# Optimization experiments

Measured on AMD Instinct MI355X. Metric: run time of the kernel, lower is better.

The kernel has to match this reference:

```python
import jax, jax.numpy as jnp
import numpy as np
import math

NEG_INF = -1e30  # stand-in for float('-inf'); softmax/logsumexp treat it identically


def _fnoise(x):
    # factorized NoisyNet transform f(x) = sign(x) * sqrt(|x|)
    return jnp.sign(x) * jnp.sqrt(jnp.abs(x))


def setup_inputs() -> dict:
    B, T, D, E = 4, 4096, 2048, 16
    key = jax.random.key(0)
    ks = jax.random.split(key, 6)
    sigma_init = 0.4 / math.sqrt(D)  # sigma_zero / sqrt(in_features)
    return {
        "mh_output": jax.random.normal(ks[0], (B, T, D), dtype=jnp.float32),
        "weight": jax.random.normal(ks[1], (E, D), dtype=jnp.float32) * 0.02,
        "sigma_weight": jnp.full((E, D), sigma_init, dtype=jnp.float32),
        "bias": jax.random.normal(ks[2], (E,), dtype=jnp.float32) * 0.02,
        "sigma_bias": jnp.full((E,), sigma_init, dtype=jnp.float32),
        "eps_in": jax.random.normal(ks[3], (D,), dtype=jnp.float32),
        "eps_out": jax.random.normal(ks[4], (E,), dtype=jnp.float32),
    }


def reference(mh_output, weight, sigma_weight, bias, sigma_bias, eps_in, eps_out):
    top_k = 2
    E = weight.shape[0]

    # NoisyFactorizedLinear: W' = W + sigma_W * (f(eps_out) f(eps_in)^T)
    f_in = _fnoise(eps_in)            # [D]
    f_out = _fnoise(eps_out)          # [E]
    w_noisy = weight + sigma_weight * (f_out[:, None] * f_in[None, :])  # [E, D]
    b_noisy = bias + sigma_bias * f_out                                 # [E]
    logits = jnp.einsum("btd,ed->bte", mh_output, w_noisy) + b_noisy    # [B,T,E]
    # dropout(p=0.125) is identity in eval mode

    top_vals, indices = jax.lax.top_k(logits, top_k)                    # [B,T,k]
    # scatter top-k back into a -inf-filled tensor == mask of selected experts
    keep = jnp.sum(jax.nn.one_hot(indices, E, dtype=jnp.bool_), axis=-2)  # [B,T,E]
    sparse_logits = jnp.where(keep, logits, NEG_INF)

    router_output = jax.nn.softmax(sparse_logits, axis=-1)

    # z-loss: mean(logsumexp(sparse_logits, -1)^2); only top-k entries survive
    lse = jax.scipy.special.logsumexp(top_vals, axis=-1)                # [B,T]
    z_loss = jnp.mean(lse ** 2)

    return router_output, indices, z_loss
```

## Files before the change

### kernel.cpp

```cpp
#include <hip/hip_runtime.h>
#include <math.h>

#define NROWS 16384
#define DDIM  2048
#define NEXP  16
#define RBLOCKS 512
#define WPB 8
#define ZN (RBLOCKS * WPB)

__device__ __forceinline__ float fnoise(float x) {
    return copysignf(sqrtf(fabsf(x)), x);
}

__device__ __forceinline__ void async_copy16(const float4* g, float4* l) {
    __builtin_amdgcn_global_load_lds(
        (const __attribute__((address_space(1))) void*)g,
        (__attribute__((address_space(3))) void*)l, 16, 0, 0);
}


__global__ void prep_kernel(const float* __restrict__ weight,
                            const float* __restrict__ sigma_weight,
                            const float* __restrict__ bias,
                            const float* __restrict__ sigma_bias,
                            const float* __restrict__ eps_in,
                            const float* __restrict__ eps_out,
                            float* __restrict__ w_noisy,
                            float* __restrict__ b_noisy) {
    int idx = blockIdx.x * blockDim.x + threadIdx.x;
    int e = idx >> 11;
    int d = idx & (DDIM - 1);
    float fi = fnoise(eps_in[d]);
    float fo = fnoise(eps_out[e]);
    w_noisy[idx] = weight[idx] + sigma_weight[idx] * fo * fi;
    if (idx < NEXP) {
        b_noisy[idx] = bias[idx] + sigma_bias[idx] * fnoise(eps_out[idx]);
    }
}

__global__ __launch_bounds__(512, 2) void router_kernel(
        const float* __restrict__ x,
        const float* __restrict__ w_noisy,
        const float* __restrict__ b_noisy,
        float* __restrict__ out_router,
        float* __restrict__ out_idx,
        float* __restrict__ zpart) {
    __shared__ float4 wlds[NEXP * 512];

    const int tid  = threadIdx.x;
    const int wv   = tid >> 6;
    const int lane = tid & 63;

    const int rowBase = blockIdx.x * 32 + wv * 4;
    const float4* xr0 = (const float4*)(x + (size_t)(rowBase + 0) * DDIM);
    const float4* xr1 = (const float4*)(x + (size_t)(rowBase + 1) * DDIM);
    const float4* xr2 = (const float4*)(x + (size_t)(rowBase + 2) * DDIM);
    const float4* xr3 = (const float4*)(x + (size_t)(rowBase + 3) * DDIM);
    const float4* wsrc = (const float4*)w_noisy;

    float acc[64];
    #pragma unroll
    for (int i = 0; i < 64; ++i) acc[i] = 0.0f;

    float4 xbuf[3][4];

    #pragma unroll
    for (int j = 0; j < 16; ++j) {
        int fb = j * 512 + wv * 64;
        async_copy16(wsrc + fb + lane, &wlds[fb]);
    }
    xbuf[0][0] = xr0[lane];       xbuf[0][1] = xr1[lane];
    xbuf[0][2] = xr2[lane];       xbuf[0][3] = xr3[lane];
    xbuf[1][0] = xr0[64 + lane];  xbuf[1][1] = xr1[64 + lane];
    xbuf[1][2] = xr2[64 + lane];  xbuf[1][3] = xr3[64 + lane];
    __syncthreads();

    #pragma unroll
    for (int c = 0; c < 8; ++c) {
        const int cur = c % 3;
        const int pre = (c + 2) % 3;
        if (c < 6) {
            int p = (c + 2) * 64 + lane;
            xbuf[pre][0] = xr0[p];
            xbuf[pre][1] = xr1[p];
            xbuf[pre][2] = xr2[p];
            xbuf[pre][3] = xr3[p];
        }
        #pragma unroll
        for (int e = 0; e < 16; ++e) {
            float4 w = wlds[e * 512 + c * 64 + lane];
            float s0 = acc[0 * 16 + e];
            float s1 = acc[1 * 16 + e];
            float s2 = acc[2 * 16 + e];
            float s3 = acc[3 * 16 + e];
            s0 = fmaf(xbuf[cur][0].x, w.x, s0); s0 = fmaf(xbuf[cur][0].y, w.y, s0);
            s0 = fmaf(xbuf[cur][0].z, w.z, s0); s0 = fmaf(xbuf[cur][0].w, w.w, s0);
            s1 = fmaf(xbuf[cur][1].x, w.x, s1); s1 = fmaf(xbuf[cur][1].y, w.y, s1);
            s1 = fmaf(xbuf[cur][1].z, w.z, s1); s1 = fmaf(xbuf[cur][1].w, w.w, s1);
            s2 = fmaf(xbuf[cur][2].x, w.x, s2); s2 = fmaf(xbuf[cur][2].y, w.y, s2);
            s2 = fmaf(xbuf[cur][2].z, w.z, s2); s2 = fmaf(xbuf[cur][2].w, w.w, s2);
            s3 = fmaf(xbuf[cur][3].x, w.x, s3); s3 = fmaf(xbuf[cur][3].y, w.y, s3);
            s3 = fmaf(xbuf[cur][3].z, w.z, s3); s3 = fmaf(xbuf[cur][3].w, w.w, s3);
            acc[0 * 16 + e] = s0;
            acc[1 * 16 + e] = s1;
            acc[2 * 16 + e] = s2;
            acc[3 * 16 + e] = s3;
        }
    }

    #pragma unroll
    for (int half = 32; half >= 1; half >>= 1) {
        #pragma unroll
        for (int i = 0; i < half; ++i) {
            bool hi = (lane & half) != 0;
            float keep = hi ? acc[i + half] : acc[i];
            float send = hi ? acc[i] : acc[i + half];
            float recv = __shfl_xor(send, half, 64);
            acc[i] = keep + recv;
        }
    }

    const int e = lane & 15;
    const int r = lane >> 4;
    const int row = rowBase + r;
    float logit = acc[0] + b_noisy[e];

    float m1 = logit; int i1 = e;
    #pragma unroll
    for (int off = 8; off >= 1; off >>= 1) {
        float om = __shfl_xor(m1, off, 64);
        int   oi = __shfl_xor(i1, off, 64);
        if (om > m1 || (om == m1 && oi < i1)) { m1 = om; i1 = oi; }
    }
    float v2 = (e == i1) ? -3.4e38f : logit;
    float m2 = v2; int i2 = e;
    #pragma unroll
    for (int off = 8; off >= 1; off >>= 1) {
        float om = __shfl_xor(m2, off, 64);
        int   oi = __shfl_xor(i2, off, 64);
        if (om > m2 || (om == m2 && oi < i2)) { m2 = om; i2 = oi; }
    }

    float t = expf(m2 - m1);
    float p1 = 1.0f / (1.0f + t);
    float val = (e == i1) ? p1 : ((e == i2) ? t * p1 : 0.0f);
    out_router[(size_t)rowBase * NEXP + lane] = val;

    if (e < 2) {
        out_idx[(size_t)row * 2 + e] = (float)((e == 0) ? i1 : i2);
    }

    float zv = 0.0f;
    if (e == 0) {
        float lse = m1 + log1pf(t);
        zv = lse * lse;
    }
    zv += __shfl_xor(zv, 16, 64);
    zv += __shfl_xor(zv, 32, 64);
    if (lane == 0) {
        zpart[blockIdx.x * WPB + wv] = zv;
    }
}

__global__ void finalize_kernel(const float* __restrict__ zpart,
                                float* __restrict__ out) {
    __shared__ float ws4[4];
    int tid = threadIdx.x;
    float s = 0.0f;
    for (int i = tid; i < ZN; i += 256) s += zpart[i];
    #pragma unroll
    for (int off = 32; off >= 1; off >>= 1) s += __shfl_xor(s, off, 64);
    if ((tid & 63) == 0) ws4[tid >> 6] = s;
    __syncthreads();
    if (tid == 0) {
        float total = ws4[0] + ws4[1] + ws4[2] + ws4[3];
        out[NROWS * NEXP + NROWS * 2] = total * (1.0f / (float)NROWS);
    }
}

extern "C" void kernel_launch(void* const* d_in, const int* in_sizes, int n_in,
                              void* d_out, int out_size, void* d_ws, size_t ws_size,
                              hipStream_t stream) {
    const float* mh      = (const float*)d_in[0];
    const float* weight  = (const float*)d_in[1];
    const float* sigw    = (const float*)d_in[2];
    const float* bias    = (const float*)d_in[3];
    const float* sigb    = (const float*)d_in[4];
    const float* eps_in  = (const float*)d_in[5];
    const float* eps_out = (const float*)d_in[6];

    float* out      = (float*)d_out;
    float* w_noisy  = (float*)d_ws;
    float* b_noisy  = w_noisy + NEXP * DDIM;
    float* zpart    = w_noisy + 32800;

    prep_kernel<<<(NEXP * DDIM) / 256, 256, 0, stream>>>(
        weight, sigw, bias, sigb, eps_in, eps_out, w_noisy, b_noisy);

    router_kernel<<<RBLOCKS, 512, 0, stream>>>(
        mh, w_noisy, b_noisy, out, out + NROWS * NEXP, zpart);

    finalize_kernel<<<1, 256, 0, stream>>>(zpart, out);
}
```

Baseline: 212.5 us.

## Process eight rows per wave with split-D weight staging in LDS

Each wave now handles 8 rows instead of 4, so each LDS weight read is reused across twice as many rows, and the grid is halved to 256 blocks. The weight matrix is staged in two halves of the D dimension: the second half is loaded asynchronously while the first is being consumed, which halves the LDS footprint. The x loads are restructured into a two-buffer ping-pong inside a non-unrolled outer loop. The cost is 128 accumulators per thread, which raises register pressure, and fewer blocks for a memory-bound stream over a large x.

```diff
diff --git a/kernel.cpp b/kernel.cpp
--- a/kernel.cpp
+++ b/kernel.cpp
@@ -4,7 +4,7 @@
 #define NROWS 16384
 #define DDIM  2048
 #define NEXP  16
-#define RBLOCKS 512
+#define RBLOCKS 256
 #define WPB 8
 #define ZN (RBLOCKS * WPB)
 
@@ -45,66 +45,74 @@
         float* __restrict__ out_router,
         float* __restrict__ out_idx,
         float* __restrict__ zpart) {
-    __shared__ float4 wlds[NEXP * 512];
+    __shared__ float4 wlds[2 * NEXP * 256];
 
     const int tid  = threadIdx.x;
     const int wv   = tid >> 6;
     const int lane = tid & 63;
 
-    const int rowBase = blockIdx.x * 32 + wv * 4;
-    const float4* xr0 = (const float4*)(x + (size_t)(rowBase + 0) * DDIM);
-    const float4* xr1 = (const float4*)(x + (size_t)(rowBase + 1) * DDIM);
-    const float4* xr2 = (const float4*)(x + (size_t)(rowBase + 2) * DDIM);
-    const float4* xr3 = (const float4*)(x + (size_t)(rowBase + 3) * DDIM);
+    const int rowBase = blockIdx.x * 64 + wv * 8;
+    const float4* xbase = (const float4*)x + (size_t)rowBase * 512;
     const float4* wsrc = (const float4*)w_noisy;
 
-    float acc[64];
-    #pragma unroll
-    for (int i = 0; i < 64; ++i) acc[i] = 0.0f;
-
-    float4 xbuf[3][4];
-
-    #pragma unroll
-    for (int j = 0; j < 16; ++j) {
+    float acc[128];
+    #pragma unroll
+    for (int i = 0; i < 128; ++i) acc[i] = 0.0f;
+
+    float4 xa[8], xb[8];
+
+    #pragma unroll
+    for (int j = 0; j < 8; ++j) {
         int fb = j * 512 + wv * 64;
-        async_copy16(wsrc + fb + lane, &wlds[fb]);
-    }
-    xbuf[0][0] = xr0[lane];       xbuf[0][1] = xr1[lane];
-    xbuf[0][2] = xr2[lane];       xbuf[0][3] = xr3[lane];
-    xbuf[1][0] = xr0[64 + lane];  xbuf[1][1] = xr1[64 + lane];
-    xbuf[1][2] = xr2[64 + lane];  xbuf[1][3] = xr3[64 + lane];
+        async_copy16(wsrc + (fb >> 8) * 512 + (fb & 255) + lane, &wlds[fb]);
+    }
+    #pragma unroll
+    for (int r = 0; r < 8; ++r) xa[r] = xbase[r * 512 + lane];
     __syncthreads();
 
     #pragma unroll
-    for (int c = 0; c < 8; ++c) {
-        const int cur = c % 3;
-        const int pre = (c + 2) % 3;
-        if (c < 6) {
-            int p = (c + 2) * 64 + lane;
-            xbuf[pre][0] = xr0[p];
-            xbuf[pre][1] = xr1[p];
-            xbuf[pre][2] = xr2[p];
-            xbuf[pre][3] = xr3[p];
-        }
+    for (int j = 0; j < 8; ++j) {
+        int fb = j * 512 + wv * 64;
+        async_copy16(wsrc + (fb >> 8) * 512 + 256 + (fb & 255) + lane,
+                     &wlds[4096 + fb]);
+    }
+
+    #pragma unroll 1
+    for (int c2 = 0; c2 < 4; ++c2) {
+        if (c2 == 2) __syncthreads();
+        const float4* wb = wlds + (c2 >> 1) * 4096 + (c2 & 1) * 128;
+        const int pe = 2 * c2 * 64 + lane;
+
+        #pragma unroll
+        for (int r = 0; r < 8; ++r) xb[r] = xbase[r * 512 + pe + 64];
+
         #pragma unroll
         for (int e = 0; e < 16; ++e) {
-            float4 w = wlds[e * 512 + c * 64 + lane];
-            float s0 = acc[0 * 16 + e];
-            float s1 = acc[1 * 16 + e];
-            float s2 = acc[2 * 16 + e];
-            float s3 = acc[3 * 16 + e];
-            s0 = fmaf(xbuf[cur][0].x, w.x, s0); s0 = fmaf(xbuf[cur][0].y, w.y, s0);
-            s0 = fmaf(xbuf[cur][0].z, w.z, s0); s0 = fmaf(xbuf[cur][0].w, w.w, s0);
-            s1 = fmaf(xbuf[cur][1].x, w.x, s1); s1 = fmaf(xbuf[cur][1].y, w.y, s1);
-            s1 = fmaf(xbuf[cur][1].z, w.z, s1); s1 = fmaf(xbuf[cur][1].w, w.w, s1);
-            s2 = fmaf(xbuf[cur][2].x, w.x, s2); s2 = fmaf(xbuf[cur][2].y, w.y, s2);
-            s2 = fmaf(xbuf[cur][2].z, w.z, s2); s2 = fmaf(xbuf[cur][2].w, w.w, s2);
-            s3 = fmaf(xbuf[cur][3].x, w.x, s3); s3 = fmaf(xbuf[cur][3].y, w.y, s3);
-            s3 = fmaf(xbuf[cur][3].z, w.z, s3); s3 = fmaf(xbuf[cur][3].w, w.w, s3);
-            acc[0 * 16 + e] = s0;
-            acc[1 * 16 + e] = s1;
-            acc[2 * 16 + e] = s2;
-            acc[3 * 16 + e] = s3;
+            float4 w = wb[e * 256 + lane];
+            #pragma unroll
+            for (int r = 0; r < 8; ++r) {
+                float s = acc[r * 16 + e];
+                s = fmaf(xa[r].x, w.x, s); s = fmaf(xa[r].y, w.y, s);
+                s = fmaf(xa[r].z, w.z, s); s = fmaf(xa[r].w, w.w, s);
+                acc[r * 16 + e] = s;
+            }
+        }
+
+        if (c2 < 3) {
+            #pragma unroll
+            for (int r = 0; r < 8; ++r) xa[r] = xbase[r * 512 + pe + 128];
+        }
+
+        #pragma unroll
+        for (int e = 0; e < 16; ++e) {
+            float4 w = wb[e * 256 + 64 + lane];
+            #pragma unroll
+            for (int r = 0; r < 8; ++r) {
+                float s = acc[r * 16 + e];
+                s = fmaf(xb[r].x, w.x, s); s = fmaf(xb[r].y, w.y, s);
+                s = fmaf(xb[r].z, w.z, s); s = fmaf(xb[r].w, w.w, s);
+                acc[r * 16 + e] = s;
+            }
         }
     }
 
@@ -115,46 +123,51 @@
             bool hi = (lane & half) != 0;
             float keep = hi ? acc[i + half] : acc[i];
             float send = hi ? acc[i] : acc[i + half];
-            float recv = __shfl_xor(send, half, 64);
-            acc[i] = keep + recv;
+            acc[i] = keep + __shfl_xor(send, half, 64);
+            float keep2 = hi ? acc[64 + i + half] : acc[64 + i];
+            float send2 = hi ? acc[64 + i] : acc[64 + i + half];
+            acc[64 + i] = keep2 + __shfl_xor(send2, half, 64);
         }
     }
 
     const int e = lane & 15;
-    const int r = lane >> 4;
-    const int row = rowBase + r;
-    float logit = acc[0] + b_noisy[e];
-
-    float m1 = logit; int i1 = e;
-    #pragma unroll
-    for (int off = 8; off >= 1; off >>= 1) {
-        float om = __shfl_xor(m1, off, 64);
-        int   oi = __shfl_xor(i1, off, 64);
-        if (om > m1 || (om == m1 && oi < i1)) { m1 = om; i1 = oi; }
-    }
-    float v2 = (e == i1) ? -3.4e38f : logit;
-    float m2 = v2; int i2 = e;
-    #pragma unroll
-    for (int off = 8; off >= 1; off >>= 1) {
-        float om = __shfl_xor(m2, off, 64);
-        int   oi = __shfl_xor(i2, off, 64);
-        if (om > m2 || (om == m2 && oi < i2)) { m2 = om; i2 = oi; }
-    }
-
-    float t = expf(m2 - m1);
-    float p1 = 1.0f / (1.0f + t);
-    float val = (e == i1) ? p1 : ((e == i2) ? t * p1 : 0.0f);
-    out_router[(size_t)rowBase * NEXP + lane] = val;
-
-    if (e < 2) {
-        out_idx[(size_t)row * 2 + e] = (float)((e == 0) ? i1 : i2);
-    }
-
+    const float bn = b_noisy[e];
     float zv = 0.0f;
-    if (e == 0) {
-        float lse = m1 + log1pf(t);
-        zv = lse * lse;
-    }
+
+    #pragma unroll
+    for (int s = 0; s < 2; ++s) {
+        float logit = acc[s * 64] + bn;
+
+        float m1 = logit; int i1 = e;
+        #pragma unroll
+        for (int off = 8; off >= 1; off >>= 1) {
+            float om = __shfl_xor(m1, off, 64);
+            int   oi = __shfl_xor(i1, off, 64);
+            if (om > m1 || (om == m1 && oi < i1)) { m1 = om; i1 = oi; }
+        }
+        float m2 = (e == i1) ? -3.4e38f : logit; int i2 = e;
+        #pragma unroll
+        for (int off = 8; off >= 1; off >>= 1) {
+            float om = __shfl_xor(m2, off, 64);
+            int   oi = __shfl_xor(i2, off, 64);
+            if (om > m2 || (om == m2 && oi < i2)) { m2 = om; i2 = oi; }
+        }
+
+        float t = expf(m2 - m1);
+        float p1 = 1.0f / (1.0f + t);
+        float val = (e == i1) ? p1 : ((e == i2) ? t * p1 : 0.0f);
+        out_router[(size_t)(rowBase + s * 4) * NEXP + lane] = val;
+
+        if (e < 2) {
+            int row = rowBase + s * 4 + (lane >> 4);
+            out_idx[(size_t)row * 2 + e] = (float)((e == 0) ? i1 : i2);
+        }
+        if (e == 0) {
+            float lse = m1 + log1pf(t);
+            zv += lse * lse;
+        }
+    }
+
     zv += __shfl_xor(zv, 16, 64);
     zv += __shfl_xor(zv, 32, 64);
     if (lane == 0) {
```

Result: slower. 238.6 us (+12.3%).
